# Optimization experiments

Measured on AMD Instinct MI355X. Metric: run time of the kernel, lower is better.

The kernel has to match this reference:

```python
import jax, jax.numpy as jnp
import numpy as np

NUM_Q = 50000
DIM_KEY = 128
DIM_VALUE = 256
DIM_HIDDEN = 512
MEM_SIZE = 50
BATCH = 128
SEQ = 2048


def setup_inputs() -> dict:
    key = jax.random.key(0)
    ks = jax.random.split(key, 12)
    inp = {
        "q": jax.random.randint(ks[0], (BATCH, SEQ), 0, NUM_Q + 1, dtype=jnp.int64 if jax.config.jax_enable_x64 else jnp.int32),
        "a": jax.random.randint(ks[1], (BATCH, SEQ), 0, 2, dtype=jnp.int64 if jax.config.jax_enable_x64 else jnp.int32),
        # learned parameters (torch Linear convention: y = x @ W.T + b)
        "key_memory": jax.random.normal(ks[2], (MEM_SIZE, DIM_KEY), jnp.float32) * 0.1,
        "value_memory": jax.random.normal(ks[3], (MEM_SIZE, DIM_VALUE), jnp.float32) * 0.1,
        "embed_table": jax.random.normal(ks[4], (NUM_Q + 1, DIM_KEY), jnp.float32) * 0.1,
        "W_erase": jax.random.normal(ks[5], (DIM_VALUE, DIM_HIDDEN), jnp.float32) * 0.05,
        "b_erase": jnp.zeros((DIM_VALUE,), jnp.float32),
        "W_add": jax.random.normal(ks[6], (DIM_VALUE, DIM_HIDDEN), jnp.float32) * 0.05,
        "b_add": jnp.zeros((DIM_VALUE,), jnp.float32),
        "W_f": jax.random.normal(ks[7], (DIM_HIDDEN, DIM_VALUE + DIM_KEY), jnp.float32) * 0.05,
        "b_f": jnp.zeros((DIM_HIDDEN,), jnp.float32),
        "W_p": jax.random.normal(ks[8], (1, DIM_HIDDEN), jnp.float32) * 0.05,
        "b_p": jnp.zeros((1,), jnp.float32),
    }
    return inp


def reference(q, a, key_memory, value_memory, embed_table, W_erase, b_erase,
              W_add, b_add, W_f, b_f, W_p, b_p):
    # NOTE: in the original torch module, read() always uses the static
    # value_memory parameter (not the per-batch updated memory), and the
    # answer sequence `a` is never used in the forward math. Hence the
    # timestep loop is embarrassingly parallel and we vectorize over t.
    q_embed = embed_table[q]                                   # [B,S,K]
    corr = jax.nn.softmax(jnp.einsum('bsk,mk->bsm', q_embed, key_memory), axis=-1)  # [B,S,M]
    read_content = jnp.einsum('bsm,mv->bsv', corr, value_memory)                    # [B,S,V]
    feat = jnp.concatenate([read_content, q_embed], axis=-1)   # [B,S,V+K]
    # dropout is identity in eval mode
    state = jax.nn.relu(jnp.einsum('bsf,hf->bsh', feat, W_f) + b_f)                 # [B,S,H]
    pred = jax.nn.sigmoid(jnp.einsum('bsh,oh->bso', state, W_p) + b_p)              # [B,S,1]
    return pred[..., 0]                                        # [B,S]
```

## Files before the change

kernel.cpp:

```cpp
#include <hip/hip_runtime.h>
#include <hip/hip_bf16.h>

#define NUM_Q_MAX 50000
#define DIM_KEY 128
#define DIM_VAL 256
#define WF_COLS 384
#define DIM_HID 512
#define MEMN    50
#define KDIM    192
#define EOFF2   64
#define NTILES  782
#define PP      72

typedef __bf16 bf16x8 __attribute__((ext_vector_type(8)));
typedef float  f32x4  __attribute__((ext_vector_type(4)));
union Frag { uint4 u; bf16x8 b; };

__device__ __forceinline__ unsigned short f2b(float x){
    unsigned u = __float_as_uint(x);
    u += 0x7fffu + ((u >> 16) & 1u);
    return (unsigned short)(u >> 16);
}
__device__ __forceinline__ unsigned pk2(float a, float b){
    return (unsigned)f2b(a) | ((unsigned)f2b(b) << 16);
}

__global__ void __launch_bounds__(64)
prep_kernel(const float* __restrict__ Wf, const float* __restrict__ Vm,
            const float* __restrict__ Kmem,
            unsigned short* __restrict__ WCt, unsigned short* __restrict__ Kbt){
    const int b = blockIdx.x, t = threadIdx.x;
    if (b < DIM_HID) {
        const int h = b, nt = h >> 4, l15 = h & 15;
        for (int j = t; j < KDIM; j += 64) {
            float val = 0.f;
            if (j < MEMN) {
                const float4* wr = (const float4*)(Wf + h * WF_COLS);
                const float4* vr = (const float4*)(Vm + j * DIM_VAL);
                float s = 0.f;
                for (int v = 0; v < DIM_VAL / 4; ++v) {
                    float4 a = wr[v], c = vr[v];
                    s += a.x*c.x + a.y*c.y + a.z*c.z + a.w*c.w;
                }
                val = s;
            } else if (j >= EOFF2) {
                val = Wf[h * WF_COLS + DIM_VAL + (j - EOFF2)];
            }
            const int ks = j >> 5, l4j = (j >> 3) & 3, e = j & 7;
            WCt[((nt * 6 + ks) * 64 + l4j * 16 + l15) * 8 + e] = f2b(val);
        }
    } else {
        for (int idx = t; idx < 4 * 4 * 64 * 8; idx += 64) {
            const int e = idx & 7, lane = (idx >> 3) & 63, ks = (idx >> 9) & 3, nt = idx >> 11;
            const int m = nt * 16 + (lane & 15), k = ks * 32 + (lane >> 4) * 8 + e;
            float v = (m < MEMN) ? Kmem[m * DIM_KEY + k] : 0.f;
            Kbt[idx] = f2b(v);
        }
    }
}

__global__ void __launch_bounds__(64, 1)
table_kernel(const float* __restrict__ emb,
             const unsigned short* __restrict__ WCt,
             const unsigned short* __restrict__ Kbt,
             const float* __restrict__ bfv, const float* __restrict__ wpv,
             const float* __restrict__ bpv, float* __restrict__ table){
    __shared__ __align__(16) unsigned short P[64][PP];
    const int lane = threadIdx.x;
    const int l15  = lane & 15;
    const int l4   = lane >> 4;
    const int q0   = blockIdx.x * 64;

    Frag ef[4][4];
    #pragma unroll
    for (int mt = 0; mt < 4; ++mt) {
        int u = q0 + mt * 16 + l15; if (u > NUM_Q_MAX) u = NUM_Q_MAX;
        const float4* eb = (const float4*)(emb + (long)u * DIM_KEY);
        #pragma unroll
        for (int ks = 0; ks < 4; ++ks) {
            float4 a = eb[ks * 8 + l4 * 2];
            float4 b = eb[ks * 8 + l4 * 2 + 1];
            uint4 w;
            w.x = pk2(a.x, a.y); w.y = pk2(a.z, a.w);
            w.z = pk2(b.x, b.y); w.w = pk2(b.z, b.w);
            ef[mt][ks].u = w;
        }
    }

    Frag bk[4][4];
    #pragma unroll
    for (int n2 = 0; n2 < 4; ++n2)
        #pragma unroll
        for (int ks = 0; ks < 4; ++ks)
            bk[n2][ks].u = *(const uint4*)&Kbt[((n2 * 4 + ks) * 64 + lane) * 8];

    #pragma unroll
    for (int mt = 0; mt < 4; ++mt) {
        f32x4 la[4];
        #pragma unroll
        for (int n2 = 0; n2 < 4; ++n2) {
            la[n2] = (f32x4){0.f, 0.f, 0.f, 0.f};
            #pragma unroll
            for (int ks = 0; ks < 4; ++ks)
                la[n2] = __builtin_amdgcn_mfma_f32_16x16x32_bf16(ef[mt][ks].b, bk[n2][ks].b, la[n2], 0, 0, 0);
        }
        float mx[4] = {-1e30f, -1e30f, -1e30f, -1e30f};
        #pragma unroll
        for (int n2 = 0; n2 < 4; ++n2) {
            const bool ok = (n2 * 16 + l15) < MEMN;
            #pragma unroll
            for (int r = 0; r < 4; ++r)
                if (ok) mx[r] = fmaxf(mx[r], la[n2][r]);
        }
        #pragma unroll
        for (int off = 1; off < 16; off <<= 1)
            #pragma unroll
            for (int r = 0; r < 4; ++r)
                mx[r] = fmaxf(mx[r], __shfl_xor(mx[r], off, 64));
        float pv[4][4], sm[4] = {0.f, 0.f, 0.f, 0.f};
        #pragma unroll
        for (int n2 = 0; n2 < 4; ++n2) {
            const bool ok = (n2 * 16 + l15) < MEMN;
            #pragma unroll
            for (int r = 0; r < 4; ++r) {
                float v = ok ? __expf(la[n2][r] - mx[r]) : 0.f;
                pv[n2][r] = v; sm[r] += v;
            }
        }
        #pragma unroll
        for (int off = 1; off < 16; off <<= 1)
            #pragma unroll
            for (int r = 0; r < 4; ++r)
                sm[r] += __shfl_xor(sm[r], off, 64);
        float iv[4];
        #pragma unroll
        for (int r = 0; r < 4; ++r) iv[r] = 1.f / sm[r];
        #pragma unroll
        for (int n2 = 0; n2 < 4; ++n2)
            #pragma unroll
            for (int r = 0; r < 4; ++r)
                P[mt * 16 + l4 * 4 + r][n2 * 16 + l15] = f2b(pv[n2][r] * iv[r]);
    }

    asm volatile("s_waitcnt lgkmcnt(0)" ::: "memory");
    __builtin_amdgcn_sched_barrier(0);

    Frag pa[4][2];
    #pragma unroll
    for (int mt = 0; mt < 4; ++mt)
        #pragma unroll
        for (int k2 = 0; k2 < 2; ++k2)
            pa[mt][k2].u = *(const uint4*)&P[mt * 16 + l15][k2 * 32 + l4 * 8];

    Frag bw[4][6];
    #pragma unroll
    for (int p = 0; p < 3; ++p)
        #pragma unroll
        for (int ks = 0; ks < 6; ++ks)
            bw[p][ks].u = *(const uint4*)&WCt[((p * 6 + ks) * 64 + lane) * 8];

    float psum[4][4];
    #pragma unroll
    for (int mt = 0; mt < 4; ++mt)
        #pragma unroll
        for (int r = 0; r < 4; ++r) psum[mt][r] = 0.f;

    #pragma unroll
    for (int nt = 0; nt < 32; ++nt) {
        if (nt + 3 < 32) {
            #pragma unroll
            for (int ks = 0; ks < 6; ++ks)
                bw[(nt + 3) & 3][ks].u = *(const uint4*)&WCt[(((nt + 3) * 6 + ks) * 64 + lane) * 8];
        }
        const float bb = bfv[nt * 16 + l15];
        const float ww = wpv[nt * 16 + l15];
        f32x4 acc[4];
        #pragma unroll
        for (int mt = 0; mt < 4; ++mt) acc[mt] = (f32x4){0.f, 0.f, 0.f, 0.f};
        #pragma unroll
        for (int k2 = 0; k2 < 2; ++k2)
            #pragma unroll
            for (int mt = 0; mt < 4; ++mt)
                acc[mt] = __builtin_amdgcn_mfma_f32_16x16x32_bf16(pa[mt][k2].b, bw[nt & 3][k2].b, acc[mt], 0, 0, 0);
        #pragma unroll
        for (int ke = 0; ke < 4; ++ke)
            #pragma unroll
            for (int mt = 0; mt < 4; ++mt)
                acc[mt] = __builtin_amdgcn_mfma_f32_16x16x32_bf16(ef[mt][ke].b, bw[nt & 3][2 + ke].b, acc[mt], 0, 0, 0);
        #pragma unroll
        for (int mt = 0; mt < 4; ++mt)
            #pragma unroll
            for (int r = 0; r < 4; ++r)
                psum[mt][r] += ww * fmaxf(acc[mt][r] + bb, 0.f);
    }

    #pragma unroll
    for (int off = 1; off < 16; off <<= 1)
        #pragma unroll
        for (int mt = 0; mt < 4; ++mt)
            #pragma unroll
            for (int r = 0; r < 4; ++r)
                psum[mt][r] += __shfl_xor(psum[mt][r], off, 64);

    if (l15 == 0) {
        const float bp0 = bpv[0];
        #pragma unroll
        for (int mt = 0; mt < 4; ++mt)
            #pragma unroll
            for (int r = 0; r < 4; ++r) {
                const int u = q0 + mt * 16 + l4 * 4 + r;
                if (u <= NUM_Q_MAX) {
                    const float s = psum[mt][r] + bp0;
                    table[u] = 1.f / (1.f + __expf(-s));
                }
            }
    }
}

__global__ void gather_kernel(const int* __restrict__ q, const float* __restrict__ table,
                              float* __restrict__ out, int n){
    int i = blockIdx.x * 256 + threadIdx.x;
    if (i < n) out[i] = table[q[i]];
}

extern "C" void kernel_launch(void* const* d_in, const int* in_sizes, int n_in,
                              void* d_out, int out_size, void* d_ws, size_t ws_size,
                              hipStream_t stream) {
    const int*   q    = (const int*)  d_in[0];
    const float* Kmem = (const float*)d_in[2];
    const float* Vmem = (const float*)d_in[3];
    const float* emb  = (const float*)d_in[4];
    const float* Wf   = (const float*)d_in[9];
    const float* bf   = (const float*)d_in[10];
    const float* wp   = (const float*)d_in[11];
    const float* bp   = (const float*)d_in[12];
    float* out = (float*)d_out;

    unsigned short* WCt   = (unsigned short*)d_ws;
    unsigned short* Kbt   = (unsigned short*)((char*)d_ws + 196608);
    float*          table = (float*)((char*)d_ws + 196608 + 16384);

    prep_kernel<<<DIM_HID + 1, 64, 0, stream>>>(Wf, Vmem, Kmem, WCt, Kbt);

    table_kernel<<<NTILES, 64, 0, stream>>>(emb, WCt, Kbt, bf, wp, bp, table);

    gather_kernel<<<(out_size + 255) / 256, 256, 0, stream>>>(q, table, out, out_size);
}
```

Baseline: 54.01 us.

## Split hidden dimension across two blocks per tile and fold bias into GEMM

The table kernel now launches two blocks per 64-query tile, each covering half of the 512 hidden units, and writes partial logit sums to a workspace buffer. The gather kernel adds the two partials plus the output bias and applies the sigmoid. The hidden bias b_f is folded into the GEMM through an unused padding column of the probability matrix that is set to 1. The W_p weights are preloaded into registers and the launch bound allows two waves per SIMD. The aim is to double the block count so the GPU is better filled and to drop the per-iteration bias and weight loads, at the cost of a slightly heavier gather and a recomputed softmax in each block.

Result: slower. 56.05 us (+3.8%).

```diff
diff --git a/kernel.cpp b/kernel.cpp
--- a/kernel.cpp
+++ b/kernel.cpp
@@ -7,9 +7,11 @@
 #define WF_COLS 384
 #define DIM_HID 512
 #define MEMN    50
+#define BIASC   50
 #define KDIM    192
 #define EOFF2   64
-#define NTILES  782
+#define QTILES  782
+#define PARTN   50048
 #define PP      72
 
 typedef __bf16 bf16x8 __attribute__((ext_vector_type(8)));
@@ -27,7 +29,7 @@
 
 __global__ void __launch_bounds__(64)
 prep_kernel(const float* __restrict__ Wf, const float* __restrict__ Vm,
-            const float* __restrict__ Kmem,
+            const float* __restrict__ Kmem, const float* __restrict__ bfv,
             unsigned short* __restrict__ WCt, unsigned short* __restrict__ Kbt){
     const int b = blockIdx.x, t = threadIdx.x;
     if (b < DIM_HID) {
@@ -43,6 +45,8 @@
                     s += a.x*c.x + a.y*c.y + a.z*c.z + a.w*c.w;
                 }
                 val = s;
+            } else if (j == BIASC) {
+                val = bfv[h];
             } else if (j >= EOFF2) {
                 val = Wf[h * WF_COLS + DIM_VAL + (j - EOFF2)];
             }
@@ -59,17 +63,18 @@
     }
 }
 
-__global__ void __launch_bounds__(64, 1)
+__global__ void __launch_bounds__(64, 2)
 table_kernel(const float* __restrict__ emb,
              const unsigned short* __restrict__ WCt,
              const unsigned short* __restrict__ Kbt,
-             const float* __restrict__ bfv, const float* __restrict__ wpv,
-             const float* __restrict__ bpv, float* __restrict__ table){
+             const float* __restrict__ wpv,
+             float* __restrict__ part){
     __shared__ __align__(16) unsigned short P[64][PP];
     const int lane = threadIdx.x;
     const int l15  = lane & 15;
     const int l4   = lane >> 4;
-    const int q0   = blockIdx.x * 64;
+    const int q0   = (blockIdx.x >> 1) * 64;
+    const int hg   = blockIdx.x & 1;
 
     Frag ef[4][4];
     #pragma unroll
@@ -136,10 +141,15 @@
         #pragma unroll
         for (int r = 0; r < 4; ++r) iv[r] = 1.f / sm[r];
         #pragma unroll
-        for (int n2 = 0; n2 < 4; ++n2)
-            #pragma unroll
-            for (int r = 0; r < 4; ++r)
-                P[mt * 16 + l4 * 4 + r][n2 * 16 + l15] = f2b(pv[n2][r] * iv[r]);
+        for (int n2 = 0; n2 < 4; ++n2) {
+            const int col = n2 * 16 + l15;
+            #pragma unroll
+            for (int r = 0; r < 4; ++r) {
+                float outv = (col < MEMN) ? pv[n2][r] * iv[r]
+                                          : (col == BIASC ? 1.0f : 0.f);
+                P[mt * 16 + l4 * 4 + r][col] = f2b(outv);
+            }
+        }
     }
 
     asm volatile("s_waitcnt lgkmcnt(0)" ::: "memory");
@@ -152,12 +162,17 @@
         for (int k2 = 0; k2 < 2; ++k2)
             pa[mt][k2].u = *(const uint4*)&P[mt * 16 + l15][k2 * 32 + l4 * 8];
 
-    Frag bw[4][6];
-    #pragma unroll
-    for (int p = 0; p < 3; ++p)
+    float wpr[16];
+    #pragma unroll
+    for (int nt = 0; nt < 16; ++nt)
+        wpr[nt] = wpv[hg * 256 + nt * 16 + l15];
+
+    Frag bw[3][6];
+    #pragma unroll
+    for (int p = 0; p < 2; ++p)
         #pragma unroll
         for (int ks = 0; ks < 6; ++ks)
-            bw[p][ks].u = *(const uint4*)&WCt[((p * 6 + ks) * 64 + lane) * 8];
+            bw[p][ks].u = *(const uint4*)&WCt[(((hg * 16 + p) * 6 + ks) * 64 + lane) * 8];
 
     float psum[4][4];
     #pragma unroll
@@ -166,14 +181,13 @@
         for (int r = 0; r < 4; ++r) psum[mt][r] = 0.f;
 
     #pragma unroll
-    for (int nt = 0; nt < 32; ++nt) {
-        if (nt + 3 < 32) {
+    for (int nt = 0; nt < 16; ++nt) {
+        if (nt + 2 < 16) {
             #pragma unroll
             for (int ks = 0; ks < 6; ++ks)
-                bw[(nt + 3) & 3][ks].u = *(const uint4*)&WCt[(((nt + 3) * 6 + ks) * 64 + lane) * 8];
-        }
-        const float bb = bfv[nt * 16 + l15];
-        const float ww = wpv[nt * 16 + l15];
+                bw[(nt + 2) % 3][ks].u =
+                    *(const uint4*)&WCt[(((hg * 16 + nt + 2) * 6 + ks) * 64 + lane) * 8];
+        }
         f32x4 acc[4];
         #pragma unroll
         for (int mt = 0; mt < 4; ++mt) acc[mt] = (f32x4){0.f, 0.f, 0.f, 0.f};
@@ -181,17 +195,17 @@
         for (int k2 = 0; k2 < 2; ++k2)
             #pragma unroll
             for (int mt = 0; mt < 4; ++mt)
-                acc[mt] = __builtin_amdgcn_mfma_f32_16x16x32_bf16(pa[mt][k2].b, bw[nt & 3][k2].b, acc[mt], 0, 0, 0);
+                acc[mt] = __builtin_amdgcn_mfma_f32_16x16x32_bf16(pa[mt][k2].b, bw[nt % 3][k2].b, acc[mt], 0, 0, 0);
         #pragma unroll
         for (int ke = 0; ke < 4; ++ke)
             #pragma unroll
             for (int mt = 0; mt < 4; ++mt)
-                acc[mt] = __builtin_amdgcn_mfma_f32_16x16x32_bf16(ef[mt][ke].b, bw[nt & 3][2 + ke].b, acc[mt], 0, 0, 0);
+                acc[mt] = __builtin_amdgcn_mfma_f32_16x16x32_bf16(ef[mt][ke].b, bw[nt % 3][2 + ke].b, acc[mt], 0, 0, 0);
         #pragma unroll
         for (int mt = 0; mt < 4; ++mt)
             #pragma unroll
             for (int r = 0; r < 4; ++r)
-                psum[mt][r] += ww * fmaxf(acc[mt][r] + bb, 0.f);
+                psum[mt][r] += wpr[nt] * fmaxf(acc[mt][r], 0.f);
     }
 
     #pragma unroll
@@ -203,24 +217,24 @@
                 psum[mt][r] += __shfl_xor(psum[mt][r], off, 64);
 
     if (l15 == 0) {
-        const float bp0 = bpv[0];
         #pragma unroll
         for (int mt = 0; mt < 4; ++mt)
             #pragma unroll
             for (int r = 0; r < 4; ++r) {
                 const int u = q0 + mt * 16 + l4 * 4 + r;
-                if (u <= NUM_Q_MAX) {
-                    const float s = psum[mt][r] + bp0;
-                    table[u] = 1.f / (1.f + __expf(-s));
-                }
-            }
-    }
-}
-
-__global__ void gather_kernel(const int* __restrict__ q, const float* __restrict__ table,
-                              float* __restrict__ out, int n){
+                if (u <= NUM_Q_MAX) part[hg * PARTN + u] = psum[mt][r];
+            }
+    }
+}
+
+__global__ void gather_kernel(const int* __restrict__ q, const float* __restrict__ part,
+                              const float* __restrict__ bpv, float* __restrict__ out, int n){
     int i = blockIdx.x * 256 + threadIdx.x;
-    if (i < n) out[i] = table[q[i]];
+    if (i < n) {
+        const int u = q[i];
+        const float s = part[u] + part[PARTN + u] + bpv[0];
+        out[i] = 1.f / (1.f + __expf(-s));
+    }
 }
 
 extern "C" void kernel_launch(void* const* d_in, const int* in_sizes, int n_in,
@@ -236,13 +250,13 @@
     const float* bp   = (const float*)d_in[12];
     float* out = (float*)d_out;
 
-    unsigned short* WCt   = (unsigned short*)d_ws;
-    unsigned short* Kbt   = (unsigned short*)((char*)d_ws + 196608);
-    float*          table = (float*)((char*)d_ws + 196608 + 16384);
-
-    prep_kernel<<<DIM_HID + 1, 64, 0, stream>>>(Wf, Vmem, Kmem, WCt, Kbt);
-
-    table_kernel<<<NTILES, 64, 0, stream>>>(emb, WCt, Kbt, bf, wp, bp, table);
-
-    gather_kernel<<<(out_size + 255) / 256, 256, 0, stream>>>(q, table, out, out_size);
-}
+    unsigned short* WCt  = (unsigned short*)d_ws;
+    unsigned short* Kbt  = (unsigned short*)((char*)d_ws + 196608);
+    float*          part = (float*)((char*)d_ws + 196608 + 16384);
+
+    prep_kernel<<<DIM_HID + 1, 64, 0, stream>>>(Wf, Vmem, Kmem, bf, WCt, Kbt);
+
+    table_kernel<<<QTILES * 2, 64, 0, stream>>>(emb, WCt, Kbt, wp, part);
+
+    gather_kernel<<<(out_size + 255) / 256, 256, 0, stream>>>(q, part, bp, out, out_size);
+}
```
